# Kernel optimization log

Measured on AMD Instinct MI355X. Metric: run time of the kernel, lower is better.

## Reference

```python
import jax, jax.numpy as jnp
import numpy as np

# Config mirrors TACO_hashed init: data_size=[1024,1024], dimensions=[[4]*5,[4]*5]
N = 262144          # number of query coordinates
DH = 256            # dim_hidden
TD = 4              # tile_dim = dimensions[0][0]
NLEV = 5            # n_levels
W0C = 30.0          # w0
DIMS = np.array([[4]*NLEV, [4]*NLEV])                 # [2, n_levels]
CUM = 1024 // np.cumprod(DIMS, axis=1)                # cum_bases per axis, [2, n_levels]


def setup_inputs() -> dict:
    key = jax.random.key(0)
    ks = jax.random.split(key, 9)
    s = 1.0 / np.sqrt(DH)
    e = TD * TD  # embedding dim = tile_dim**2 = 16
    return {
        "coords": jax.random.randint(ks[0], (N, 2), 0, 1024, dtype=jnp.int32),
        "W0": jax.random.normal(ks[1], (2, DH), jnp.float32) * (1.0 / np.sqrt(2.0)),
        "b0": jnp.zeros((DH,), jnp.float32),
        "Wh": jax.random.normal(ks[2], (3, DH, DH), jnp.float32) * s,  # hidden SIREN linears
        "bh": jnp.zeros((3, DH), jnp.float32),
        "emb": jax.random.normal(ks[3], (NLEV - 1, e, e), jnp.float32),      # per-level embedding tables
        "modW": jax.random.normal(ks[4], (NLEV - 1, e, DH), jnp.float32) * (1.0 / np.sqrt(e)),  # modulator linears (no bias)
        "Wl": jax.random.normal(ks[5], (DH, 3), jnp.float32) * s,  # last_layer
        "bl": jnp.zeros((3,), jnp.float32),
    }


def reference(coords, W0, b0, Wh, bh, emb, modW, Wl, bl):
    dims = jnp.asarray(DIMS.T)   # [n_levels, 2]
    cum = jnp.asarray(CUM.T)     # [n_levels, 2]
    # decompose_coords: per-level bitwise-style div/mod  -> [N, n_levels, 2]
    lv = (coords[:, None, :] // cum[None]) % dims[None]
    # modulator indices for levels 1..n_levels-1: idx = y*tile_dim + x  -> [N, n_levels-1]
    idx = lv[:, 1:, 1] * TD + lv[:, 1:, 0]
    # SIREN input is level-0 coords as float (faithful to the source)
    x = lv[:, 0, :].astype(jnp.float32) @ W0 + b0
    x = x + W0C * (emb[0][idx[:, 0]] @ modW[0])
    x = jnp.sin(W0C * x)
    for j in range(3):
        x = x @ Wh[j] + bh[j]
        x = x + W0C * (emb[j + 1][idx[:, j + 1]] @ modW[j + 1])
        x = jnp.sin(W0C * x)
    return x @ Wl + bl
```

## Files before the change

### kernel.cpp

```cpp
#include <hip/hip_runtime.h>
#include <hip/hip_bf16.h>
#include <math.h>


typedef float  f32x4  __attribute__((ext_vector_type(4)));
typedef int    i32x4  __attribute__((ext_vector_type(4)));
typedef __bf16 bf16x8 __attribute__((ext_vector_type(8)));

__device__ __forceinline__ float fbar(float v) {
  asm volatile("" : "+v"(v));
  return v;
}

__device__ __forceinline__ unsigned short f2bf_rne(float x) {
  unsigned u = __float_as_uint(x);
  unsigned r = (u + 0x7fffu + ((u >> 16) & 1u)) >> 16;
  return (unsigned short)r;
}

__device__ __forceinline__ void gload16(const void* g, void* l) {
  __builtin_amdgcn_global_load_lds(
      (const __attribute__((address_space(1))) unsigned*)g,
      (__attribute__((address_space(3))) unsigned*)l, 16, 0, 0);
}

__device__ __forceinline__ float sin30(float x) {
  const float Ch = 4.774648189544678f;
  const float Cl = 1.0321218e-07f;
  float revh = x * Ch;
  fbar(revh);
  float e    = __builtin_fmaf(x, Ch, -revh);
  float revl = __builtin_fmaf(x, Cl, e);
  float k2   = __builtin_rintf(revh + revh);
  float g    = __builtin_fmaf(k2, -0.5f, revh) + revl;
  float g2 = g * g;
  float r = -15.0946f;
  r = __builtin_fmaf(r, g2, 42.0601f);
  r = __builtin_fmaf(r, g2, -76.70585f);
  r = __builtin_fmaf(r, g2, 81.6052492f);
  r = __builtin_fmaf(r, g2, -41.341702f);
  r = __builtin_fmaf(r, g2, 6.2831853f);
  float s = g * r;
  int ki = (int)k2;
  return __uint_as_float(__float_as_uint(s) ^ ((unsigned)(ki & 1) << 31));
}

__device__ __forceinline__ void sincos30(float x, float* so, float* co) {
  const float Ch = 4.774648189544678f;
  const float Cl = 1.0321218e-07f;
  float revh = x * Ch;
  fbar(revh);
  float e    = __builtin_fmaf(x, Ch, -revh);
  float revl = __builtin_fmaf(x, Cl, e);
  float k2   = __builtin_rintf(revh + revh);
  float g    = __builtin_fmaf(k2, -0.5f, revh) + revl;
  float u = g * g;
  float sr = -15.0946f;
  sr = __builtin_fmaf(sr, u, 42.0601f);
  sr = __builtin_fmaf(sr, u, -76.70585f);
  sr = __builtin_fmaf(sr, u, 81.6052492f);
  sr = __builtin_fmaf(sr, u, -41.341702f);
  sr = __builtin_fmaf(sr, u, 6.2831853f);
  float s = g * sr;
  float cr = -26.4259f;
  cr = __builtin_fmaf(cr, u, 60.2446f);
  cr = __builtin_fmaf(cr, u, -85.4568f);
  cr = __builtin_fmaf(cr, u, 64.9393940f);
  cr = __builtin_fmaf(cr, u, -19.7392088f);
  float c = __builtin_fmaf(cr, u, 1.0f);
  int ki = (int)k2;
  unsigned sgn = ((unsigned)(ki & 1)) << 31;
  *so = __uint_as_float(__float_as_uint(s) ^ sgn);
  *co = __uint_as_float(__float_as_uint(c) ^ sgn);
}

__global__ void k_prep(const float* __restrict__ emb, const float* __restrict__ modW,
                       float* __restrict__ Mf, float* __restrict__ T2C,
                       float* __restrict__ T2S, const float* __restrict__ Wl,
                       unsigned* __restrict__ B2u, const float* __restrict__ W2,
                       unsigned short* __restrict__ B2T) {
  int b = blockIdx.x, d = threadIdx.x;
  if (b < 64) {
    int j = b >> 4, i = b & 15;
    float acc = 0.0f;
#pragma unroll
    for (int e = 0; e < 16; ++e)
      acc = __builtin_fmaf(emb[j * 256 + i * 16 + e], modW[(j * 16 + e) * 256 + d], acc);
    Mf[b * 256 + d] = acc;
    if (j == 2) {
      float pm = fbar(30.0f * acc);
      float s, c;
      sincos30(pm, &s, &c);
      T2C[i * 256 + d] = c;
      T2S[i * 256 + d] = s;
    } else if (j == 3) {
      float pm = fbar(30.0f * acc);
      float s, c;
      sincos30(pm, &s, &c);
      int p = (d & 0xC0) | ((d & 15) << 2) | ((d >> 4) & 3);
#pragma unroll
      for (int q = 0; q < 3; ++q) {
        float w = Wl[d * 3 + q];
        unsigned ts = (unsigned)f2bf_rne(s * w);
        unsigned tc = (unsigned)f2bf_rne(c * w);
        B2u[(i * 3 + q) * 256 + p] = (tc << 16) | ts;
      }
    }
  } else {
    int col = b - 64, k = d;
    float w = W2[k * 256 + col];
    unsigned short hi = f2bf_rne(w);
    float hif = __uint_as_float((unsigned)hi << 16);
    unsigned short lo = f2bf_rne(w - hif);
    B2T[col * 768 + k] = hi;
    B2T[col * 768 + 256 + k] = lo;
    B2T[col * 768 + 512 + k] = hi;
  }
}

__global__ void __launch_bounds__(512) k_h123(
    const float* __restrict__ W0, const float* __restrict__ b0,
    const float* __restrict__ Wh0, const float* __restrict__ bh0,
    const float* __restrict__ W1, const float* __restrict__ b1,
    const float* __restrict__ Mf, const float* __restrict__ T2C,
    const float* __restrict__ T2S,
    unsigned short* __restrict__ Ah, unsigned short* __restrict__ Al) {
  __shared__ float xs1[256];
  __shared__ float xs2[8][256];
  int b = blockIdx.x, t = threadIdx.x;
  int d = t & 255, hf = t >> 8;
  int c1 = b >> 1;
  int i1base = (b & 1) * 8 + hf * 4;
  if (hf == 0) {
    float lvx = (float)((c1 >> 6) & 3), lvy = (float)((c1 >> 4) & 3);
    int i0 = c1 & 15;
    float tt = fbar(lvx * W0[d]);
    tt = __builtin_fmaf(lvy, W0[256 + d], tt);
    tt = fbar(tt + b0[d]);
    float p = fbar(30.0f * Mf[i0 * 256 + d]);
    float xv = fbar(tt + p);
    xs1[d] = sinf(fbar(30.0f * xv));
  }
  __syncthreads();
  float acc = 0.0f;
  for (int k = 0; k < 256; ++k)
    acc = __builtin_fmaf(xs1[k], Wh0[k * 256 + d], acc);
  float t2 = fbar(acc + bh0[d]);
#pragma unroll
  for (int rr = 0; rr < 4; ++rr) {
    int i1 = i1base + rr;
    float pp = fbar(30.0f * Mf[4096 + i1 * 256 + d]);
    float x2 = fbar(t2 + pp);
    xs2[hf * 4 + rr][d] = sin30(x2);
  }
  __syncthreads();
  float acc3[4] = {0.f, 0.f, 0.f, 0.f};
  for (int k = 0; k < 256; ++k) {
    float w = W1[k * 256 + d];
#pragma unroll
    for (int r = 0; r < 4; ++r)
      acc3[r] = __builtin_fmaf(xs2[hf * 4 + r][k], w, acc3[r]);
  }
  float tcv[16], tsv[16];
#pragma unroll
  for (int i = 0; i < 16; ++i) {
    tcv[i] = T2C[i * 256 + d];
    tsv[i] = T2S[i * 256 + d];
  }
  float bias = b1[d];
#pragma unroll
  for (int rr = 0; rr < 4; ++rr) {
    float targ = fbar(acc3[rr] + bias);
    float sT, cT;
    sincos30(targ, &sT, &cT);
    int c3base = (b * 8 + hf * 4 + rr) * 16;
#pragma unroll
    for (int i = 0; i < 16; ++i) {
      float hv = __builtin_fmaf(cT, tsv[i], sT * tcv[i]);
      unsigned short hi = f2bf_rne(hv);
      float hif = __uint_as_float((unsigned)hi << 16);
      unsigned short lo = f2bf_rne(hv - hif);
      size_t o = (size_t)(c3base + i) * 256 + d;
      Ah[o] = hi;
      Al[o] = lo;
    }
  }
}

__global__ void __launch_bounds__(512, 1) k_gemm(
    const unsigned short* __restrict__ Ah, const unsigned short* __restrict__ Al,
    const unsigned short* __restrict__ B2T, const float* __restrict__ b2,
    unsigned* __restrict__ SC) {
  __shared__ unsigned short As[2][128 * 32];
  __shared__ unsigned short Bs[2][256 * 32];
  const int t = threadIdx.x;
  const int lane = t & 63, wid = t >> 6;
  const int l15 = lane & 15, l4 = lane >> 4;
  const int wm = (wid >> 2) * 64;
  const int wn = (wid & 3) * 64;
  const size_t r0 = (size_t)blockIdx.x * 128;

  const int arow = t >> 2, apart = t & 3;
  const int gpart = (apart - ((arow >> 1) & 3)) & 3;
  const size_t bcol0 = t >> 2, bcol1 = (t >> 2) + 128;

  f32x4 acc[4][4];
#pragma unroll
  for (int rf = 0; rf < 4; ++rf)
#pragma unroll
    for (int cf = 0; cf < 4; ++cf) acc[rf][cf] = (f32x4){0.f, 0.f, 0.f, 0.f};

#define STAGE(c, bb)                                                         \
  {                                                                          \
    const unsigned short* asrc = ((c) >= 16) ? Al : Ah;                      \
    gload16(asrc + ((r0 + arow) << 8) + ((c) & 7) * 32 + gpart * 8,          \
            (void*)(&As[bb][wid * 512]));                                    \
    gload16(B2T + bcol0 * 768 + (c) * 32 + gpart * 8,                        \
            (void*)(&Bs[bb][wid * 512]));                                    \
    gload16(B2T + bcol1 * 768 + (c) * 32 + gpart * 8,                        \
            (void*)(&Bs[bb][(wid + 8) * 512]));                              \
  }

  STAGE(0, 0);
  __syncthreads();
  const int sp8 = ((l4 + (l15 >> 1)) & 3) * 8;
#pragma unroll 1
  for (int c = 0; c < 24; ++c) {
    int cur = c & 1;
    if (c < 23) STAGE(c + 1, cur ^ 1);
    bf16x8 af[4], bfr[4];
#pragma unroll
    for (int rf = 0; rf < 4; ++rf)
      af[rf] = __builtin_bit_cast(
          bf16x8, *(const i32x4*)(&As[cur][(wm + rf * 16 + l15) * 32 + sp8]));
#pragma unroll
    for (int cf = 0; cf < 4; ++cf)
      bfr[cf] = __builtin_bit_cast(
          bf16x8, *(const i32x4*)(&Bs[cur][(wn + cf * 16 + l15) * 32 + sp8]));
#pragma unroll
    for (int rf = 0; rf < 4; ++rf)
#pragma unroll
      for (int cf = 0; cf < 4; ++cf)
        acc[rf][cf] = __builtin_amdgcn_mfma_f32_16x16x32_bf16(
            af[rf], bfr[cf], acc[rf][cf], 0, 0, 0);
    __syncthreads();
  }
#undef STAGE

  float bias[4];
#pragma unroll
  for (int cf = 0; cf < 4; ++cf) bias[cf] = b2[wn + cf * 16 + l15];
#pragma unroll
  for (int rf = 0; rf < 4; ++rf) {
#pragma unroll
    for (int j = 0; j < 4; ++j) {
      unsigned pk[4];
#pragma unroll
      for (int cf = 0; cf < 4; ++cf) {
        float g = acc[rf][cf][j] + bias[cf];
        float s, c;
        sincos30(g, &s, &c);
        pk[cf] = ((unsigned)f2bf_rne(s) << 16) | (unsigned)f2bf_rne(c);
      }
      size_t row = r0 + wm + rf * 16 + l4 * 4 + j;
      *(i32x4*)(SC + row * 256 + wn + l15 * 4) =
          (i32x4){(int)pk[0], (int)pk[1], (int)pk[2], (int)pk[3]};
    }
  }
}

__global__ void __launch_bounds__(512, 1) k_ugemm(
    const unsigned short* __restrict__ SCb, const unsigned* __restrict__ B2u,
    float* __restrict__ U) {
  __shared__ unsigned short As[128 * 40];
  __shared__ unsigned Bs[48 * 260];
  const int t = threadIdx.x;
  const int lane = t & 63, wid = t >> 6;
  const int l15 = lane & 15, l4 = lane >> 4;
  const int wm = wid * 16;
  const size_t r0 = (size_t)blockIdx.x * 128;

#pragma unroll
  for (int i = 0; i < 24; ++i) {
    int lin = t + i * 512;
    int col = lin >> 8, kp = lin & 255;
    Bs[col * 260 + kp] = B2u[lin];
  }

  const int s_row = t >> 2, s_part = t & 3;
  f32x4 acc[3];
#pragma unroll
  for (int cf = 0; cf < 3; ++cf) acc[cf] = (f32x4){0.f, 0.f, 0.f, 0.f};

  i32x4 ra = *(const i32x4*)(SCb + (r0 + s_row) * 512 + s_part * 8);
#pragma unroll 1
  for (int c = 0; c < 16; ++c) {
    *(i32x4*)(As + s_row * 40 + s_part * 8) = ra;
    __syncthreads();
    if (c < 15)
      ra = *(const i32x4*)(SCb + (r0 + s_row) * 512 + (c + 1) * 32 + s_part * 8);
    bf16x8 af = __builtin_bit_cast(
        bf16x8, *(const i32x4*)(As + (wm + l15) * 40 + l4 * 8));
#pragma unroll
    for (int cf = 0; cf < 3; ++cf) {
      bf16x8 bfr = __builtin_bit_cast(
          bf16x8, *(const i32x4*)(Bs + (cf * 16 + l15) * 260 + c * 16 + l4 * 4));
      acc[cf] = __builtin_amdgcn_mfma_f32_16x16x32_bf16(af, bfr, acc[cf], 0, 0, 0);
    }
    __syncthreads();
  }

#pragma unroll
  for (int cf = 0; cf < 3; ++cf) {
    size_t rbase = r0 + wm + l4 * 4;
#pragma unroll
    for (int j = 0; j < 4; ++j)
      U[(rbase + j) * 48 + cf * 16 + l15] = acc[cf][j];
  }
}

__global__ void k_gather(const int* __restrict__ coords, const float* __restrict__ U,
                         const float* __restrict__ bl, float* __restrict__ out, int N) {
  int n = blockIdx.x * blockDim.x + threadIdx.x;
  if (n >= N) return;
  int x = coords[2 * n], y = coords[2 * n + 1];
  int c1 = ((x >> 8) & 3) * 64 + ((y >> 8) & 3) * 16 +
           (((y >> 6) & 3) * 4 + ((x >> 6) & 3));
  int i1 = ((y >> 4) & 3) * 4 + ((x >> 4) & 3);
  int i2 = ((y >> 2) & 3) * 4 + ((x >> 2) & 3);
  int i3 = (y & 3) * 4 + (x & 3);
  int c3 = (c1 * 16 + i1) * 16 + i2;
  const float* up = U + (size_t)c3 * 48 + i3 * 3;
  out[n * 3 + 0] = up[0] + bl[0];
  out[n * 3 + 1] = up[1] + bl[1];
  out[n * 3 + 2] = up[2] + bl[2];
}

__global__ void k_direct(const int* __restrict__ coords, const float* __restrict__ W0,
                         const float* __restrict__ b0, const float* __restrict__ Wh,
                         const float* __restrict__ bh, const float* __restrict__ emb,
                         const float* __restrict__ modW, const float* __restrict__ Wl,
                         const float* __restrict__ bl, float* __restrict__ out) {
  __shared__ float xs[256];
  __shared__ float red[256];
  int n = blockIdx.x, d = threadIdx.x;
  int x = coords[2 * n], y = coords[2 * n + 1];
  float lvx = (float)((x >> 8) & 3), lvy = (float)((y >> 8) & 3);
  int idx[4];
  idx[0] = ((y >> 6) & 3) * 4 + ((x >> 6) & 3);
  idx[1] = ((y >> 4) & 3) * 4 + ((x >> 4) & 3);
  idx[2] = ((y >> 2) & 3) * 4 + ((x >> 2) & 3);
  idx[3] = (y & 3) * 4 + (x & 3);
  float m = 0.0f;
#pragma unroll
  for (int e = 0; e < 16; ++e)
    m = __builtin_fmaf(emb[idx[0] * 16 + e], modW[e * 256 + d], m);
  float t = fbar(lvx * W0[d]);
  t = __builtin_fmaf(lvy, W0[256 + d], t);
  t = fbar(t + b0[d]);
  float p = fbar(30.0f * m);
  float xv = fbar(t + p);
  xs[d] = sinf(fbar(30.0f * xv));
  __syncthreads();
  for (int j = 0; j < 3; ++j) {
    float acc = 0.0f;
    for (int k = 0; k < 256; ++k)
      acc = __builtin_fmaf(xs[k], Wh[j * 65536 + k * 256 + d], acc);
    float tt = fbar(acc + bh[j * 256 + d]);
    m = 0.0f;
#pragma unroll
    for (int e = 0; e < 16; ++e)
      m = __builtin_fmaf(emb[(j + 1) * 256 + idx[j + 1] * 16 + e],
                         modW[((j + 1) * 16 + e) * 256 + d], m);
    p = fbar(30.0f * m);
    xv = fbar(tt + p);
    float h = sinf(fbar(30.0f * xv));
    __syncthreads();
    xs[d] = h;
    __syncthreads();
  }
  for (int q = 0; q < 3; ++q) {
    red[d] = xs[d] * Wl[d * 3 + q];
    __syncthreads();
    for (int s = 128; s > 0; s >>= 1) {
      if (d < s) red[d] += red[d + s];
      __syncthreads();
    }
    if (d == 0) out[n * 3 + q] = red[0] + bl[q];
    __syncthreads();
  }
}

extern "C" void kernel_launch(void* const* d_in, const int* in_sizes, int n_in,
                              void* d_out, int out_size, void* d_ws, size_t ws_size,
                              hipStream_t stream) {
  const int*   coords = (const int*)d_in[0];
  const float* W0   = (const float*)d_in[1];
  const float* b0   = (const float*)d_in[2];
  const float* Wh   = (const float*)d_in[3];
  const float* bh   = (const float*)d_in[4];
  const float* emb  = (const float*)d_in[5];
  const float* modW = (const float*)d_in[6];
  const float* Wl   = (const float*)d_in[7];
  const float* bl   = (const float*)d_in[8];
  float* out = (float*)d_out;
  const int N = in_sizes[0] / 2;

  const size_t OFF_MF  = 0;
  const size_t OFF_B2T = 65536;
  const size_t OFF_AH  = 458752;
  const size_t OFF_AL  = 34013184;
  const size_t OFF_SC  = 67567616;
  const size_t OFF_B2  = 134676480;
  const size_t OFF_T2C = 134774784;
  const size_t OFF_T2S = 134791168;
  const size_t OFF_U   = OFF_AH;
  const size_t NEED    = 134807552;

  if (ws_size >= NEED) {
    char* ws = (char*)d_ws;
    float*          Mf  = (float*)(ws + OFF_MF);
    unsigned short* B2T = (unsigned short*)(ws + OFF_B2T);
    unsigned short* Ahp = (unsigned short*)(ws + OFF_AH);
    unsigned short* Alp = (unsigned short*)(ws + OFF_AL);
    unsigned*       SC  = (unsigned*)(ws + OFF_SC);
    unsigned*       B2u = (unsigned*)(ws + OFF_B2);
    float*          T2C = (float*)(ws + OFF_T2C);
    float*          T2S = (float*)(ws + OFF_T2S);
    float*          U   = (float*)(ws + OFF_U);

    k_prep<<<320, 256, 0, stream>>>(emb, modW, Mf, T2C, T2S, Wl, B2u,
                                    Wh + 131072, B2T);
    k_h123<<<512, 512, 0, stream>>>(W0, b0, Wh, bh, Wh + 65536, bh + 256, Mf,
                                    T2C, T2S, Ahp, Alp);
    k_gemm<<<512, 512, 0, stream>>>(Ahp, Alp, B2T, bh + 512, SC);
    k_ugemm<<<512, 512, 0, stream>>>((const unsigned short*)SC, B2u, U);
    k_gather<<<(N + 255) / 256, 256, 0, stream>>>(coords, U, bl, out, N);
  } else {
    k_direct<<<N, 256, 0, stream>>>(coords, W0, b0, Wh, bh, emb, modW, Wl, bl, out);
  }
}
```

Before: 104.3 us.

## Fuse level-3 sin-sum expansion into GEMM A-operand generation

Instead of having k_h123 materialise the 64MB hi/lo bf16 A matrices (4096 rows × 16 level-3 tiles), it now stores only per-row sin/cos pairs. The GEMM kernel rebuilds the A fragments in registers with the angle-addition formula, splits them into hi/lo bf16, and streams only B through LDS. B2T is re-laid out so each 32-wide k chunk is stored as hi, lo, hi consecutively, matching the new chunk order. This removes a large global write and re-read of intermediates, at the cost of extra ALU and per-lane global loads inside the GEMM loop.

```diff
diff --git a/kernel.cpp b/kernel.cpp
--- a/kernel.cpp
+++ b/kernel.cpp
@@ -75,8 +75,8 @@
 }
 
 __global__ void k_prep(const float* __restrict__ emb, const float* __restrict__ modW,
-                       float* __restrict__ Mf, float* __restrict__ T2C,
-                       float* __restrict__ T2S, const float* __restrict__ Wl,
+                       float* __restrict__ Mf, float2* __restrict__ TCS,
+                       const float* __restrict__ Wl,
                        unsigned* __restrict__ B2u, const float* __restrict__ W2,
                        unsigned short* __restrict__ B2T) {
   int b = blockIdx.x, d = threadIdx.x;
@@ -91,8 +91,7 @@
       float pm = fbar(30.0f * acc);
       float s, c;
       sincos30(pm, &s, &c);
-      T2C[i * 256 + d] = c;
-      T2S[i * 256 + d] = s;
+      TCS[i * 256 + d] = make_float2(c, s);
     } else if (j == 3) {
       float pm = fbar(30.0f * acc);
       float s, c;
@@ -112,9 +111,10 @@
     unsigned short hi = f2bf_rne(w);
     float hif = __uint_as_float((unsigned)hi << 16);
     unsigned short lo = f2bf_rne(w - hif);
-    B2T[col * 768 + k] = hi;
-    B2T[col * 768 + 256 + k] = lo;
-    B2T[col * 768 + 512 + k] = hi;
+    int base = col * 768 + (k >> 5) * 96 + (k & 31);
+    B2T[base] = hi;
+    B2T[base + 32] = lo;
+    B2T[base + 64] = hi;
   }
 }
 
@@ -122,9 +122,7 @@
     const float* __restrict__ W0, const float* __restrict__ b0,
     const float* __restrict__ Wh0, const float* __restrict__ bh0,
     const float* __restrict__ W1, const float* __restrict__ b1,
-    const float* __restrict__ Mf, const float* __restrict__ T2C,
-    const float* __restrict__ T2S,
-    unsigned short* __restrict__ Ah, unsigned short* __restrict__ Al) {
+    const float* __restrict__ Mf, float2* __restrict__ STC) {
   __shared__ float xs1[256];
   __shared__ float xs2[8][256];
   int b = blockIdx.x, t = threadIdx.x;
@@ -161,37 +159,21 @@
     for (int r = 0; r < 4; ++r)
       acc3[r] = __builtin_fmaf(xs2[hf * 4 + r][k], w, acc3[r]);
   }
-  float tcv[16], tsv[16];
-#pragma unroll
-  for (int i = 0; i < 16; ++i) {
-    tcv[i] = T2C[i * 256 + d];
-    tsv[i] = T2S[i * 256 + d];
-  }
   float bias = b1[d];
 #pragma unroll
   for (int rr = 0; rr < 4; ++rr) {
     float targ = fbar(acc3[rr] + bias);
     float sT, cT;
     sincos30(targ, &sT, &cT);
-    int c3base = (b * 8 + hf * 4 + rr) * 16;
-#pragma unroll
-    for (int i = 0; i < 16; ++i) {
-      float hv = __builtin_fmaf(cT, tsv[i], sT * tcv[i]);
-      unsigned short hi = f2bf_rne(hv);
-      float hif = __uint_as_float((unsigned)hi << 16);
-      unsigned short lo = f2bf_rne(hv - hif);
-      size_t o = (size_t)(c3base + i) * 256 + d;
-      Ah[o] = hi;
-      Al[o] = lo;
-    }
+    int c2 = b * 8 + hf * 4 + rr;
+    STC[c2 * 256 + d] = make_float2(sT, cT);
   }
 }
 
 __global__ void __launch_bounds__(512, 1) k_gemm(
-    const unsigned short* __restrict__ Ah, const unsigned short* __restrict__ Al,
+    const float2* __restrict__ STC, const float2* __restrict__ TCS,
     const unsigned short* __restrict__ B2T, const float* __restrict__ b2,
     unsigned* __restrict__ SC) {
-  __shared__ unsigned short As[2][128 * 32];
   __shared__ unsigned short Bs[2][256 * 32];
   const int t = threadIdx.x;
   const int lane = t & 63, wid = t >> 6;
@@ -199,6 +181,7 @@
   const int wm = (wid >> 2) * 64;
   const int wn = (wid & 3) * 64;
   const size_t r0 = (size_t)blockIdx.x * 128;
+  const int c2base = (int)(r0 >> 4) + (wid >> 2) * 4;
 
   const int arow = t >> 2, apart = t & 3;
   const int gpart = (apart - ((arow >> 1) & 3)) & 3;
@@ -210,42 +193,83 @@
 #pragma unroll
     for (int cf = 0; cf < 4; ++cf) acc[rf][cf] = (f32x4){0.f, 0.f, 0.f, 0.f};
 
-#define STAGE(c, bb)                                                         \
+#define STAGEB(c, bb)                                                        \
   {                                                                          \
-    const unsigned short* asrc = ((c) >= 16) ? Al : Ah;                      \
-    gload16(asrc + ((r0 + arow) << 8) + ((c) & 7) * 32 + gpart * 8,          \
-            (void*)(&As[bb][wid * 512]));                                    \
     gload16(B2T + bcol0 * 768 + (c) * 32 + gpart * 8,                        \
             (void*)(&Bs[bb][wid * 512]));                                    \
     gload16(B2T + bcol1 * 768 + (c) * 32 + gpart * 8,                        \
             (void*)(&Bs[bb][(wid + 8) * 512]));                              \
   }
 
-  STAGE(0, 0);
+  STAGEB(0, 0);
   __syncthreads();
   const int sp8 = ((l4 + (l15 >> 1)) & 3) * 8;
+  const int d0 = l4 * 8;
+
 #pragma unroll 1
-  for (int c = 0; c < 24; ++c) {
-    int cur = c & 1;
-    if (c < 23) STAGE(c + 1, cur ^ 1);
-    bf16x8 af[4], bfr[4];
-#pragma unroll
-    for (int rf = 0; rf < 4; ++rf)
-      af[rf] = __builtin_bit_cast(
-          bf16x8, *(const i32x4*)(&As[cur][(wm + rf * 16 + l15) * 32 + sp8]));
-#pragma unroll
-    for (int cf = 0; cf < 4; ++cf)
-      bfr[cf] = __builtin_bit_cast(
-          bf16x8, *(const i32x4*)(&Bs[cur][(wn + cf * 16 + l15) * 32 + sp8]));
-#pragma unroll
-    for (int rf = 0; rf < 4; ++rf)
+  for (int q = 0; q < 8; ++q) {
+    int dq = q * 32 + d0;
+    f32x4 tc2[4];
+    {
+      const f32x4* tp = (const f32x4*)(TCS + l15 * 256 + dq);
+#pragma unroll
+      for (int p = 0; p < 4; ++p) tc2[p] = tp[p];
+    }
+    f32x4 sc2[4][4];
+#pragma unroll
+    for (int rf = 0; rf < 4; ++rf) {
+      const f32x4* sp = (const f32x4*)(STC + (size_t)(c2base + rf) * 256 + dq);
+#pragma unroll
+      for (int p = 0; p < 4; ++p) sc2[rf][p] = sp[p];
+    }
+    bf16x8 afh[4], afl[4];
+#pragma unroll
+    for (int rf = 0; rf < 4; ++rf) {
+      unsigned ph[4], pl[4];
+#pragma unroll
+      for (int p = 0; p < 4; ++p) {
+        float h0 = __builtin_fmaf(sc2[rf][p][1], tc2[p][1], sc2[rf][p][0] * tc2[p][0]);
+        float h1 = __builtin_fmaf(sc2[rf][p][3], tc2[p][3], sc2[rf][p][2] * tc2[p][2]);
+        unsigned hi0 = f2bf_rne(h0), hi1 = f2bf_rne(h1);
+        float lo0 = h0 - __uint_as_float(hi0 << 16);
+        float lo1 = h1 - __uint_as_float(hi1 << 16);
+        ph[p] = (hi1 << 16) | hi0;
+        pl[p] = ((unsigned)f2bf_rne(lo1) << 16) | (unsigned)f2bf_rne(lo0);
+      }
+      afh[rf] = __builtin_bit_cast(
+          bf16x8, (i32x4){(int)ph[0], (int)ph[1], (int)ph[2], (int)ph[3]});
+      afl[rf] = __builtin_bit_cast(
+          bf16x8, (i32x4){(int)pl[0], (int)pl[1], (int)pl[2], (int)pl[3]});
+    }
+#pragma unroll
+    for (int s = 0; s < 3; ++s) {
+      int c = q * 3 + s;
+      int cur = c & 1;
+      if (c < 23) STAGEB(c + 1, cur ^ 1);
+      bf16x8 bfr[4];
 #pragma unroll
       for (int cf = 0; cf < 4; ++cf)
-        acc[rf][cf] = __builtin_amdgcn_mfma_f32_16x16x32_bf16(
-            af[rf], bfr[cf], acc[rf][cf], 0, 0, 0);
-    __syncthreads();
-  }
-#undef STAGE
+        bfr[cf] = __builtin_bit_cast(
+            bf16x8, *(const i32x4*)(&Bs[cur][(wn + cf * 16 + l15) * 32 + sp8]));
+      if (s < 2) {
+#pragma unroll
+        for (int rf = 0; rf < 4; ++rf)
+#pragma unroll
+          for (int cf = 0; cf < 4; ++cf)
+            acc[rf][cf] = __builtin_amdgcn_mfma_f32_16x16x32_bf16(
+                afh[rf], bfr[cf], acc[rf][cf], 0, 0, 0);
+      } else {
+#pragma unroll
+        for (int rf = 0; rf < 4; ++rf)
+#pragma unroll
+          for (int cf = 0; cf < 4; ++cf)
+            acc[rf][cf] = __builtin_amdgcn_mfma_f32_16x16x32_bf16(
+                afl[rf], bfr[cf], acc[rf][cf], 0, 0, 0);
+      }
+      __syncthreads();
+    }
+  }
+#undef STAGEB
 
   float bias[4];
 #pragma unroll
@@ -408,32 +432,28 @@
 
   const size_t OFF_MF  = 0;
   const size_t OFF_B2T = 65536;
-  const size_t OFF_AH  = 458752;
-  const size_t OFF_AL  = 34013184;
-  const size_t OFF_SC  = 67567616;
-  const size_t OFF_B2  = 134676480;
-  const size_t OFF_T2C = 134774784;
-  const size_t OFF_T2S = 134791168;
-  const size_t OFF_U   = OFF_AH;
-  const size_t NEED    = 134807552;
+  const size_t OFF_STC = 458752;
+  const size_t OFF_TCS = 8847360;
+  const size_t OFF_B2  = 8880128;
+  const size_t OFF_SC  = 8978432;
+  const size_t OFF_U   = 76087296;
+  const size_t NEED    = 88670208;
 
   if (ws_size >= NEED) {
     char* ws = (char*)d_ws;
     float*          Mf  = (float*)(ws + OFF_MF);
     unsigned short* B2T = (unsigned short*)(ws + OFF_B2T);
-    unsigned short* Ahp = (unsigned short*)(ws + OFF_AH);
-    unsigned short* Alp = (unsigned short*)(ws + OFF_AL);
+    float2*         STC = (float2*)(ws + OFF_STC);
+    float2*         TCS = (float2*)(ws + OFF_TCS);
+    unsigned*       B2u = (unsigned*)(ws + OFF_B2);
     unsigned*       SC  = (unsigned*)(ws + OFF_SC);
-    unsigned*       B2u = (unsigned*)(ws + OFF_B2);
-    float*          T2C = (float*)(ws + OFF_T2C);
-    float*          T2S = (float*)(ws + OFF_T2S);
     float*          U   = (float*)(ws + OFF_U);
 
-    k_prep<<<320, 256, 0, stream>>>(emb, modW, Mf, T2C, T2S, Wl, B2u,
+    k_prep<<<320, 256, 0, stream>>>(emb, modW, Mf, TCS, Wl, B2u,
                                     Wh + 131072, B2T);
     k_h123<<<512, 512, 0, stream>>>(W0, b0, Wh, bh, Wh + 65536, bh + 256, Mf,
-                                    T2C, T2S, Ahp, Alp);
-    k_gemm<<<512, 512, 0, stream>>>(Ahp, Alp, B2T, bh + 512, SC);
+                                    STC);
+    k_gemm<<<512, 512, 0, stream>>>(STC, TCS, B2T, bh + 512, SC);
     k_ugemm<<<512, 512, 0, stream>>>((const unsigned short*)SC, B2u, U);
     k_gather<<<(N + 255) / 256, 256, 0, stream>>>(coords, U, bl, out, N);
   } else {
```

Result: slower. 132.6 us (+27.1%).

## Fuse final-layer projection GEMM into hidden GEMM epilogue via shared memory

Applied to the files above, without the earlier changes.

The separate k_ugemm kernel is removed. The sin/cos activation tile is now written to a swizzled shared-memory buffer in two 64-row halves and multiplied by the last-layer weights inside k_gemm. The two K halves are split across waves and reduced through shared memory. This drops the global write and re-read of the large intermediate SC buffer and one kernel launch, at the cost of more shared memory per block, extra barriers, and B operands read directly from global memory.

```diff
diff --git a/kernel.cpp b/kernel.cpp
--- a/kernel.cpp
+++ b/kernel.cpp
@@ -190,9 +190,15 @@
 __global__ void __launch_bounds__(512, 1) k_gemm(
     const unsigned short* __restrict__ Ah, const unsigned short* __restrict__ Al,
     const unsigned short* __restrict__ B2T, const float* __restrict__ b2,
-    unsigned* __restrict__ SC) {
-  __shared__ unsigned short As[2][128 * 32];
-  __shared__ unsigned short Bs[2][256 * 32];
+    const unsigned* __restrict__ B2u, float* __restrict__ U) {
+  __shared__ __align__(16) char pool[77824];
+  unsigned short* As0 = (unsigned short*)pool;
+  unsigned short* As1 = (unsigned short*)(pool + 8192);
+  unsigned short* Bs0 = (unsigned short*)(pool + 16384);
+  unsigned short* Bs1 = (unsigned short*)(pool + 32768);
+  unsigned* SCl = (unsigned*)pool;
+  float*    Pp  = (float*)(pool + 65536);
+
   const int t = threadIdx.x;
   const int lane = t & 63, wid = t >> 6;
   const int l15 = lane & 15, l4 = lane >> 4;
@@ -213,12 +219,14 @@
 #define STAGE(c, bb)                                                         \
   {                                                                          \
     const unsigned short* asrc = ((c) >= 16) ? Al : Ah;                      \
+    unsigned short* asd = (bb) ? As1 : As0;                                  \
+    unsigned short* bsd = (bb) ? Bs1 : Bs0;                                  \
     gload16(asrc + ((r0 + arow) << 8) + ((c) & 7) * 32 + gpart * 8,          \
-            (void*)(&As[bb][wid * 512]));                                    \
+            (void*)(asd + wid * 512));                                       \
     gload16(B2T + bcol0 * 768 + (c) * 32 + gpart * 8,                        \
-            (void*)(&Bs[bb][wid * 512]));                                    \
+            (void*)(bsd + wid * 512));                                       \
     gload16(B2T + bcol1 * 768 + (c) * 32 + gpart * 8,                        \
-            (void*)(&Bs[bb][(wid + 8) * 512]));                              \
+            (void*)(bsd + (wid + 8) * 512));                                 \
   }
 
   STAGE(0, 0);
@@ -228,15 +236,17 @@
   for (int c = 0; c < 24; ++c) {
     int cur = c & 1;
     if (c < 23) STAGE(c + 1, cur ^ 1);
+    const unsigned short* Asc = cur ? As1 : As0;
+    const unsigned short* Bsc = cur ? Bs1 : Bs0;
     bf16x8 af[4], bfr[4];
 #pragma unroll
     for (int rf = 0; rf < 4; ++rf)
       af[rf] = __builtin_bit_cast(
-          bf16x8, *(const i32x4*)(&As[cur][(wm + rf * 16 + l15) * 32 + sp8]));
+          bf16x8, *(const i32x4*)(Asc + (wm + rf * 16 + l15) * 32 + sp8));
 #pragma unroll
     for (int cf = 0; cf < 4; ++cf)
       bfr[cf] = __builtin_bit_cast(
-          bf16x8, *(const i32x4*)(&Bs[cur][(wn + cf * 16 + l15) * 32 + sp8]));
+          bf16x8, *(const i32x4*)(Bsc + (wn + cf * 16 + l15) * 32 + sp8));
 #pragma unroll
     for (int rf = 0; rf < 4; ++rf)
 #pragma unroll
@@ -250,72 +260,68 @@
   float bias[4];
 #pragma unroll
   for (int cf = 0; cf < 4; ++cf) bias[cf] = b2[wn + cf * 16 + l15];
-#pragma unroll
-  for (int rf = 0; rf < 4; ++rf) {
-#pragma unroll
-    for (int j = 0; j < 4; ++j) {
-      unsigned pk[4];
-#pragma unroll
-      for (int cf = 0; cf < 4; ++cf) {
-        float g = acc[rf][cf][j] + bias[cf];
-        float s, c;
-        sincos30(g, &s, &c);
-        pk[cf] = ((unsigned)f2bf_rne(s) << 16) | (unsigned)f2bf_rne(c);
+  const int g = wid & 3, kh = wid >> 2;
+
+#pragma unroll 1
+  for (int h = 0; h < 2; ++h) {
+    if (wm == h * 64) {
+#pragma unroll
+      for (int rf = 0; rf < 4; ++rf) {
+#pragma unroll
+        for (int j = 0; j < 4; ++j) {
+          unsigned pk[4];
+#pragma unroll
+          for (int cf = 0; cf < 4; ++cf) {
+            float gg = acc[rf][cf][j] + bias[cf];
+            float s, c;
+            sincos30(gg, &s, &c);
+            pk[cf] = ((unsigned)f2bf_rne(s) << 16) | (unsigned)f2bf_rne(c);
+          }
+          int rowL = rf * 16 + l4 * 4 + j;
+          int p0 = (wn + l15 * 4) ^ ((rowL & 7) << 2);
+          *(i32x4*)(SCl + rowL * 256 + p0) =
+              (i32x4){(int)pk[0], (int)pk[1], (int)pk[2], (int)pk[3]};
+        }
       }
-      size_t row = r0 + wm + rf * 16 + l4 * 4 + j;
-      *(i32x4*)(SC + row * 256 + wn + l15 * 4) =
-          (i32x4){(int)pk[0], (int)pk[1], (int)pk[2], (int)pk[3]};
-    }
-  }
-}
-
-__global__ void __launch_bounds__(512, 1) k_ugemm(
-    const unsigned short* __restrict__ SCb, const unsigned* __restrict__ B2u,
-    float* __restrict__ U) {
-  __shared__ unsigned short As[128 * 40];
-  __shared__ unsigned Bs[48 * 260];
-  const int t = threadIdx.x;
-  const int lane = t & 63, wid = t >> 6;
-  const int l15 = lane & 15, l4 = lane >> 4;
-  const int wm = wid * 16;
-  const size_t r0 = (size_t)blockIdx.x * 128;
-
-#pragma unroll
-  for (int i = 0; i < 24; ++i) {
-    int lin = t + i * 512;
-    int col = lin >> 8, kp = lin & 255;
-    Bs[col * 260 + kp] = B2u[lin];
-  }
-
-  const int s_row = t >> 2, s_part = t & 3;
-  f32x4 acc[3];
-#pragma unroll
-  for (int cf = 0; cf < 3; ++cf) acc[cf] = (f32x4){0.f, 0.f, 0.f, 0.f};
-
-  i32x4 ra = *(const i32x4*)(SCb + (r0 + s_row) * 512 + s_part * 8);
-#pragma unroll 1
-  for (int c = 0; c < 16; ++c) {
-    *(i32x4*)(As + s_row * 40 + s_part * 8) = ra;
-    __syncthreads();
-    if (c < 15)
-      ra = *(const i32x4*)(SCb + (r0 + s_row) * 512 + (c + 1) * 32 + s_part * 8);
-    bf16x8 af = __builtin_bit_cast(
-        bf16x8, *(const i32x4*)(As + (wm + l15) * 40 + l4 * 8));
-#pragma unroll
-    for (int cf = 0; cf < 3; ++cf) {
-      bf16x8 bfr = __builtin_bit_cast(
-          bf16x8, *(const i32x4*)(Bs + (cf * 16 + l15) * 260 + c * 16 + l4 * 4));
-      acc[cf] = __builtin_amdgcn_mfma_f32_16x16x32_bf16(af, bfr, acc[cf], 0, 0, 0);
-    }
-    __syncthreads();
-  }
-
-#pragma unroll
-  for (int cf = 0; cf < 3; ++cf) {
-    size_t rbase = r0 + wm + l4 * 4;
-#pragma unroll
-    for (int j = 0; j < 4; ++j)
-      U[(rbase + j) * 48 + cf * 16 + l15] = acc[cf][j];
+    }
+    __syncthreads();
+    f32x4 uacc[3];
+#pragma unroll
+    for (int cf = 0; cf < 3; ++cf) uacc[cf] = (f32x4){0.f, 0.f, 0.f, 0.f};
+    {
+      int rowL = g * 16 + l15;
+      int swz = (rowL & 7) << 2;
+#pragma unroll
+      for (int cc = 0; cc < 8; ++cc) {
+        int c = kh * 8 + cc;
+        bf16x8 af = __builtin_bit_cast(
+            bf16x8, *(const i32x4*)(SCl + rowL * 256 + ((c * 16 + l4 * 4) ^ swz)));
+#pragma unroll
+        for (int cf = 0; cf < 3; ++cf) {
+          bf16x8 bfr = __builtin_bit_cast(
+              bf16x8, *(const i32x4*)(B2u + (cf * 16 + l15) * 256 + c * 16 + l4 * 4));
+          uacc[cf] = __builtin_amdgcn_mfma_f32_16x16x32_bf16(af, bfr, uacc[cf], 0, 0, 0);
+        }
+      }
+    }
+    if (kh == 1) {
+#pragma unroll
+      for (int cf = 0; cf < 3; ++cf)
+        *(f32x4*)(Pp + ((g * 3 + cf) * 64 + lane) * 4) = uacc[cf];
+    }
+    __syncthreads();
+    if (kh == 0) {
+#pragma unroll
+      for (int cf = 0; cf < 3; ++cf) {
+        f32x4 part = *(const f32x4*)(Pp + ((g * 3 + cf) * 64 + lane) * 4);
+        uacc[cf] += part;
+        size_t rbase = r0 + h * 64 + g * 16 + l4 * 4;
+#pragma unroll
+        for (int j = 0; j < 4; ++j)
+          U[(rbase + j) * 48 + cf * 16 + l15] = uacc[cf][j];
+      }
+    }
+    __syncthreads();
   }
 }
 
@@ -410,11 +416,10 @@
   const size_t OFF_B2T = 65536;
   const size_t OFF_AH  = 458752;
   const size_t OFF_AL  = 34013184;
-  const size_t OFF_SC  = 67567616;
+  const size_t OFF_U   = 67567616;
   const size_t OFF_B2  = 134676480;
   const size_t OFF_T2C = 134774784;
   const size_t OFF_T2S = 134791168;
-  const size_t OFF_U   = OFF_AH;
   const size_t NEED    = 134807552;
 
   if (ws_size >= NEED) {
@@ -423,18 +428,16 @@
     unsigned short* B2T = (unsigned short*)(ws + OFF_B2T);
     unsigned short* Ahp = (unsigned short*)(ws + OFF_AH);
     unsigned short* Alp = (unsigned short*)(ws + OFF_AL);
-    unsigned*       SC  = (unsigned*)(ws + OFF_SC);
+    float*          U   = (float*)(ws + OFF_U);
     unsigned*       B2u = (unsigned*)(ws + OFF_B2);
     float*          T2C = (float*)(ws + OFF_T2C);
     float*          T2S = (float*)(ws + OFF_T2S);
-    float*          U   = (float*)(ws + OFF_U);
 
     k_prep<<<320, 256, 0, stream>>>(emb, modW, Mf, T2C, T2S, Wl, B2u,
                                     Wh + 131072, B2T);
     k_h123<<<512, 512, 0, stream>>>(W0, b0, Wh, bh, Wh + 65536, bh + 256, Mf,
                                     T2C, T2S, Ahp, Alp);
-    k_gemm<<<512, 512, 0, stream>>>(Ahp, Alp, B2T, bh + 512, SC);
-    k_ugemm<<<512, 512, 0, stream>>>((const unsigned short*)SC, B2u, U);
+    k_gemm<<<512, 512, 0, stream>>>(Ahp, Alp, B2T, bh + 512, B2u, U);
     k_gather<<<(N + 255) / 256, 256, 0, stream>>>(coords, U, bl, out, N);
   } else {
     k_direct<<<N, 256, 0, stream>>>(coords, W0, b0, Wh, bh, emb, modW, Wl, bl, out);
```

New measurement: 119.8 us. 14.9% more time.
